# Kernel tuning notes

Hardware: AMD Instinct MI355X
Metric: run time of the kernel (lower is better)

Reference implementation:

```python
import jax, jax.numpy as jnp
import numpy as np

B, S, D = 8, 2048, 512
FF = 2048
E = 8

def setup_inputs() -> dict:
    key = jax.random.key(0)
    ks = jax.random.split(key, 7)
    s = 1.0 / np.sqrt(D)
    sf = 1.0 / np.sqrt(FF)
    return {
        "x":  jax.random.normal(ks[0], (B, S, D), dtype=jnp.float32),
        "Wg": jax.random.uniform(ks[1], (D, E), jnp.float32, -s, s),
        "bg": jax.random.uniform(ks[2], (E,), jnp.float32, -s, s),
        "W1": jax.random.uniform(ks[3], (E, D, FF), jnp.float32, -s, s),
        "b1": jax.random.uniform(ks[4], (E, FF), jnp.float32, -s, s),
        "W2": jax.random.uniform(ks[5], (E, FF, D), jnp.float32, -sf, sf),
        "b2": jax.random.uniform(ks[6], (E, D), jnp.float32, -sf, sf),
    }

def reference(x, Wg, bg, W1, b1, W2, b2):
    b, s, d = x.shape
    xf = x.reshape(-1, d)                      # [T, D]
    logits = xf @ Wg + bg                      # [T, E]
    probs = jax.nn.softmax(logits, axis=-1)
    pmax = jnp.max(probs, axis=-1)             # [T]
    routes = jnp.argmax(probs, axis=-1)        # [T] int
    xs = xf * pmax[:, None]                    # scale tokens by router prob
    # per-expert FFN over all tokens, select the routed expert's output
    out_tok = jnp.zeros_like(xf)
    for e in range(E):
        h = jax.nn.relu(xs @ W1[e] + b1[e])    # [T, FF]
        y = h @ W2[e] + b2[e]                  # [T, D]
        out_tok = jnp.where((routes == e)[:, None], y, out_tok)
    # torch.cat of per-expert nonzero-index gathers == tokens stably sorted by expert id
    order = jnp.argsort(routes)                # jnp.argsort is stable
    return out_tok[order].reshape(b, s, d)
```

## Files before the change

### kernel.cpp

```cpp
#include <hip/hip_runtime.h>
#include <hip/hip_bf16.h>

constexpr int TTOK  = 16384;
constexpr int DDIM  = 512;
constexpr int FFDIM = 2048;
constexpr int NEXP  = 8;
constexpr int GB_TOK = 64;
constexpr int NGB    = TTOK / GB_TOK;
constexpr int MAXTILES = TTOK / 128 + NEXP;

typedef __attribute__((ext_vector_type(8))) short short8_t;
typedef __attribute__((ext_vector_type(4))) float f32x4_t;

__device__ __forceinline__ unsigned short f2bf(float f) {
    union { float f; unsigned u; } v; v.f = f;
    return (unsigned short)((v.u + 0x7fffu + ((v.u >> 16) & 1u)) >> 16);
}

__device__ __forceinline__ void gl_lds16(const void* g, void* l) {
    __builtin_amdgcn_global_load_lds(
        (const __attribute__((address_space(1))) void*)g,
        (__attribute__((address_space(3))) void*)l,
        16, 0, 0);
}

__global__ __launch_bounds__(256) void transpose_cvt(const float* __restrict__ src,
                                                     unsigned short* __restrict__ dst,
                                                     int R, int C) {
    __shared__ float tile[32][33];
    int e = blockIdx.z;
    int c0 = blockIdx.x * 32;
    int r0 = blockIdx.y * 32;
    const float* s = src + (size_t)e * R * C;
    unsigned short* d = dst + (size_t)e * R * C;
    int tx = threadIdx.x, ty = threadIdx.y;
    #pragma unroll
    for (int i = 0; i < 4; i++)
        tile[ty + 8 * i][tx] = s[(size_t)(r0 + ty + 8 * i) * C + c0 + tx];
    __syncthreads();
    #pragma unroll
    for (int i = 0; i < 4; i++)
        d[(size_t)(c0 + ty + 8 * i) * R + r0 + tx] = f2bf(tile[tx][ty + 8 * i]);
}

__global__ __launch_bounds__(256) void gate_kernel(const float* __restrict__ x,
                                                   const float* __restrict__ Wg,
                                                   const float* __restrict__ bg,
                                                   int* __restrict__ route,
                                                   float* __restrict__ pmax,
                                                   int* __restrict__ blockCounts) {
    __shared__ int cnt[NEXP];
    __shared__ float bgs[NEXP];
    int tid = threadIdx.x;
    if (tid < NEXP) { cnt[tid] = 0; bgs[tid] = bg[tid]; }
    __syncthreads();
    int wave = tid >> 6, lane = tid & 63;
    float w[8][8];
    #pragma unroll
    for (int jj = 0; jj < 8; jj++) {
        float4 a = *(const float4*)(Wg + (size_t)(lane * 8 + jj) * NEXP);
        float4 b = *(const float4*)(Wg + (size_t)(lane * 8 + jj) * NEXP + 4);
        w[jj][0] = a.x; w[jj][1] = a.y; w[jj][2] = a.z; w[jj][3] = a.w;
        w[jj][4] = b.x; w[jj][5] = b.y; w[jj][6] = b.z; w[jj][7] = b.w;
    }
    int tbase = blockIdx.x * GB_TOK + wave * 16;
    for (int it = 0; it < 16; it++) {
        int t = tbase + it;
        float4 xa = *(const float4*)(x + (size_t)t * DDIM + lane * 8);
        float4 xb = *(const float4*)(x + (size_t)t * DDIM + lane * 8 + 4);
        float xs[8] = {xa.x, xa.y, xa.z, xa.w, xb.x, xb.y, xb.z, xb.w};
        double acc[NEXP];
        #pragma unroll
        for (int e = 0; e < NEXP; e++) acc[e] = 0.0;
        #pragma unroll
        for (int jj = 0; jj < 8; jj++) {
            double xv = (double)xs[jj];
            #pragma unroll
            for (int e = 0; e < NEXP; e++) acc[e] += xv * (double)w[jj][e];
        }
        #pragma unroll
        for (int off = 32; off > 0; off >>= 1) {
            #pragma unroll
            for (int e = 0; e < NEXP; e++) acc[e] += __shfl_down(acc[e], off);
        }
        if (lane == 0) {
            double l[NEXP];
            #pragma unroll
            for (int e = 0; e < NEXP; e++) l[e] = acc[e] + (double)bgs[e];
            int r = 0; double lm = l[0];
            #pragma unroll
            for (int e = 1; e < NEXP; e++) if (l[e] > lm) { lm = l[e]; r = e; }
            double s = 0.0;
            #pragma unroll
            for (int e = 0; e < NEXP; e++) s += exp(l[e] - lm);
            route[t] = r;
            pmax[t] = (float)(1.0 / s);
            atomicAdd(&cnt[r], 1);
        }
    }
    __syncthreads();
    if (tid < NEXP) blockCounts[blockIdx.x * NEXP + tid] = cnt[tid];
}

__global__ __launch_bounds__(NGB) void scan_kernel(const int* __restrict__ blockCounts,
                                                   int* __restrict__ blockOffsets,
                                                   int* __restrict__ segPrefix,
                                                   int* __restrict__ tilePrefix) {
    __shared__ int sc[NGB][NEXP];
    __shared__ int base[NEXP + 1];
    int b = threadIdx.x;
    int c[NEXP];
    #pragma unroll
    for (int e = 0; e < NEXP; e++) { c[e] = blockCounts[b * NEXP + e]; sc[b][e] = c[e]; }
    __syncthreads();
    for (int off = 1; off < NGB; off <<= 1) {
        int t[NEXP];
        if (b >= off) {
            #pragma unroll
            for (int e = 0; e < NEXP; e++) t[e] = sc[b - off][e];
        }
        __syncthreads();
        if (b >= off) {
            #pragma unroll
            for (int e = 0; e < NEXP; e++) sc[b][e] += t[e];
        }
        __syncthreads();
    }
    if (b == 0) {
        int s = 0;
        #pragma unroll
        for (int e = 0; e < NEXP; e++) { base[e] = s; s += sc[NGB - 1][e]; }
        base[NEXP] = s;
        for (int e = 0; e <= NEXP; e++) segPrefix[e] = base[e];
        int tp = 0;
        tilePrefix[0] = 0;
        for (int e = 0; e < NEXP; e++) {
            tp += (sc[NGB - 1][e] + 127) / 128;
            tilePrefix[e + 1] = tp;
        }
    }
    __syncthreads();
    #pragma unroll
    for (int e = 0; e < NEXP; e++)
        blockOffsets[b * NEXP + e] = base[e] + sc[b][e] - c[e];
}

__global__ __launch_bounds__(256) void scatter_kernel(const float* __restrict__ x,
                                                      const int* __restrict__ route,
                                                      const float* __restrict__ pmax,
                                                      const int* __restrict__ blockOffsets,
                                                      unsigned short* __restrict__ Xs) {
    __shared__ int dstL[GB_TOK];
    __shared__ float pmL[GB_TOK];
    int tid = threadIdx.x;
    int bb = blockIdx.x;
    if (tid < 64) {
        int t = bb * GB_TOK + tid;
        int r = route[t];
        unsigned long long ltmask = (tid == 0) ? 0ull : ((~0ull) >> (64 - tid));
        int rank = 0;
        #pragma unroll
        for (int e = 0; e < NEXP; e++) {
            unsigned long long m = __ballot(r == e);
            if (r == e) rank = __popcll(m & ltmask);
        }
        dstL[tid] = blockOffsets[bb * NEXP + r] + rank;
        pmL[tid] = pmax[t];
    }
    __syncthreads();
    int wave = tid >> 6, lane = tid & 63;
    for (int rr = 0; rr < 16; rr++) {
        int rowl = wave * 16 + rr;
        int t = bb * GB_TOK + rowl;
        float pm = pmL[rowl];
        const float4* xr = (const float4*)(x + (size_t)t * DDIM) + lane * 2;
        float4 a = xr[0], b = xr[1];
        union { short8_t v; unsigned short s[8]; } o;
        o.s[0] = f2bf(a.x * pm); o.s[1] = f2bf(a.y * pm);
        o.s[2] = f2bf(a.z * pm); o.s[3] = f2bf(a.w * pm);
        o.s[4] = f2bf(b.x * pm); o.s[5] = f2bf(b.y * pm);
        o.s[6] = f2bf(b.z * pm); o.s[7] = f2bf(b.w * pm);
        *(short8_t*)(Xs + (size_t)dstL[rowl] * DDIM + lane * 8) = o.v;
    }
}

template <bool RELU, bool BIAS, typename OutT>
__global__ __launch_bounds__(256) void gemm_seg(const unsigned short* __restrict__ A,
                                                const unsigned short* __restrict__ Bt,
                                                const float* __restrict__ bias,
                                                OutT* __restrict__ C,
                                                const int* __restrict__ segPrefix,
                                                const int* __restrict__ tilePrefix,
                                                int K, int N, int kLen) {
    int t = blockIdx.x;
    if (t >= tilePrefix[NEXP]) return;
    int e = 0;
    #pragma unroll
    for (int i = 1; i <= NEXP; i++) e += (t >= tilePrefix[i]) ? 1 : 0;
    int seg1 = segPrefix[e + 1];
    int m0 = segPrefix[e] + (t - tilePrefix[e]) * 128;
    int n0 = blockIdx.y * 128;
    int kc0 = blockIdx.z * kLen;
    C += (size_t)blockIdx.z * TTOK * N;

    __shared__ unsigned short As[2 * 4096];
    __shared__ unsigned short Bs[2 * 4096];

    int tid = threadIdx.x, wave = tid >> 6, lane = tid & 63;
    const unsigned short* Bte = Bt + (size_t)e * N * K;

    int srow = lane >> 2;
    int scol = (lane & 3) * 8;

    f32x4_t acc[4][4];
    #pragma unroll
    for (int i = 0; i < 4; i++)
        #pragma unroll
        for (int j = 0; j < 4; j++) acc[i][j] = (f32x4_t){0.f, 0.f, 0.f, 0.f};

    int wm = (wave & 1) * 64;
    int wn = (wave >> 1) * 64;
    int frow = lane & 15;
    int fk = (lane >> 4) * 8;

    for (int kc = 0; kc < kLen; kc += 64) {
        int kg = kc0 + kc;
        #pragma unroll
        for (int p = 0; p < 2; p++) {
            #pragma unroll
            for (int i = 0; i < 2; i++) {
                int reg = wave * 2 + i;
                int arow = m0 + reg * 16 + srow;
                arow = arow < TTOK ? arow : TTOK - 1;
                gl_lds16(A + (size_t)arow * K + kg + p * 32 + scol, &As[p * 4096 + reg * 512]);
                int brow = n0 + reg * 16 + srow;
                gl_lds16(Bte + (size_t)brow * K + kg + p * 32 + scol, &Bs[p * 4096 + reg * 512]);
            }
        }
        __syncthreads();
        #pragma unroll
        for (int p = 0; p < 2; p++) {
            short8_t af[4], bfr[4];
            #pragma unroll
            for (int i = 0; i < 4; i++)
                af[i] = *(const short8_t*)&As[p * 4096 + (wm + i * 16 + frow) * 32 + fk];
            #pragma unroll
            for (int j = 0; j < 4; j++)
                bfr[j] = *(const short8_t*)&Bs[p * 4096 + (wn + j * 16 + frow) * 32 + fk];
            #pragma unroll
            for (int i = 0; i < 4; i++)
                #pragma unroll
                for (int j = 0; j < 4; j++)
                    acc[i][j] = __builtin_amdgcn_mfma_f32_16x16x32_bf16(af[i], bfr[j], acc[i][j], 0, 0, 0);
        }
        __syncthreads();
    }

    int quad = lane >> 4;
    int colb = lane & 15;
    #pragma unroll
    for (int i = 0; i < 4; i++) {
        #pragma unroll
        for (int j = 0; j < 4; j++) {
            int col = n0 + wn + j * 16 + colb;
            float bv = BIAS ? bias[(size_t)e * N + col] : 0.0f;
            #pragma unroll
            for (int r = 0; r < 4; r++) {
                int row = m0 + wm + i * 16 + quad * 4 + r;
                if (row < seg1) {
                    float v = acc[i][j][r] + bv;
                    if (RELU) v = fmaxf(v, 0.0f);
                    if constexpr (sizeof(OutT) == 2) {
                        C[(size_t)row * N + col] = (OutT)f2bf(v);
                    } else {
                        C[(size_t)row * N + col] = v;
                    }
                }
            }
        }
    }
}

__global__ __launch_bounds__(256) void reduce_add(const float* __restrict__ part,
                                                  const float* __restrict__ b2,
                                                  const int* __restrict__ segPrefix,
                                                  float* __restrict__ out) {
    __shared__ int sp[NEXP + 1];
    if (threadIdx.x <= NEXP) sp[threadIdx.x] = segPrefix[threadIdx.x];
    __syncthreads();
    int wave = threadIdx.x >> 6, lane = threadIdx.x & 63;
    int row = blockIdx.x * 4 + wave;
    int e = 0;
    #pragma unroll
    for (int i = 1; i < NEXP; i++) e += (row >= sp[i]) ? 1 : 0;
    const float4* p0 = (const float4*)(part + (size_t)row * DDIM) + lane * 2;
    const float4* p1 = (const float4*)(part + (size_t)(TTOK + row) * DDIM) + lane * 2;
    const float4* bv = (const float4*)(b2 + (size_t)e * DDIM) + lane * 2;
    float4* o = (float4*)(out + (size_t)row * DDIM) + lane * 2;
    #pragma unroll
    for (int k = 0; k < 2; k++) {
        float4 a = p0[k], b = p1[k], c = bv[k];
        o[k] = make_float4(a.x + b.x + c.x, a.y + b.y + c.y,
                           a.z + b.z + c.z, a.w + b.w + c.w);
    }
}

extern "C" void kernel_launch(void* const* d_in, const int* in_sizes, int n_in,
                              void* d_out, int out_size, void* d_ws, size_t ws_size,
                              hipStream_t stream) {
    const float* x  = (const float*)d_in[0];
    const float* Wg = (const float*)d_in[1];
    const float* bg = (const float*)d_in[2];
    const float* W1 = (const float*)d_in[3];
    const float* b1 = (const float*)d_in[4];
    const float* W2 = (const float*)d_in[5];
    const float* b2 = (const float*)d_in[6];
    float* out = (float*)d_out;

    char* ws = (char*)d_ws;
    size_t off = 0;
    auto alloc = [&](size_t bytes) -> char* {
        char* p = ws + off;
        off += (bytes + 255) & ~(size_t)255;
        return p;
    };
    unsigned short* W1T = (unsigned short*)alloc((size_t)NEXP * DDIM * FFDIM * 2);
    unsigned short* W2T = (unsigned short*)alloc((size_t)NEXP * DDIM * FFDIM * 2);
    unsigned short* Xs  = (unsigned short*)alloc((size_t)TTOK * DDIM * 2);
    unsigned short* H   = (unsigned short*)alloc((size_t)TTOK * FFDIM * 2);
    int*   route        = (int*)alloc((size_t)TTOK * 4);
    float* pmaxArr      = (float*)alloc((size_t)TTOK * 4);
    int*   blockCounts  = (int*)alloc((size_t)NGB * NEXP * 4);
    int*   blockOffsets = (int*)alloc((size_t)NGB * NEXP * 4);
    int*   segPrefix    = (int*)alloc((size_t)(NEXP + 1) * 4);
    int*   tilePrefix   = (int*)alloc((size_t)(NEXP + 1) * 4);
    size_t baseBytes = off;
    float* part = (float*)alloc((size_t)2 * TTOK * DDIM * 4);
    bool doSplit = (off <= ws_size);
    if (!doSplit) off = baseBytes;

    transpose_cvt<<<dim3(FFDIM / 32, DDIM / 32, NEXP), dim3(32, 8), 0, stream>>>(W1, W1T, DDIM, FFDIM);
    transpose_cvt<<<dim3(DDIM / 32, FFDIM / 32, NEXP), dim3(32, 8), 0, stream>>>(W2, W2T, FFDIM, DDIM);
    gate_kernel<<<NGB, 256, 0, stream>>>(x, Wg, bg, route, pmaxArr, blockCounts);
    scan_kernel<<<1, NGB, 0, stream>>>(blockCounts, blockOffsets, segPrefix, tilePrefix);
    scatter_kernel<<<NGB, 256, 0, stream>>>(x, route, pmaxArr, blockOffsets, Xs);
    gemm_seg<true, true, unsigned short><<<dim3(MAXTILES, FFDIM / 128, 1), 256, 0, stream>>>(
        Xs, W1T, b1, H, segPrefix, tilePrefix, DDIM, FFDIM, DDIM);
    if (doSplit) {
        gemm_seg<false, false, float><<<dim3(MAXTILES, DDIM / 128, 2), 256, 0, stream>>>(
            H, W2T, nullptr, part, segPrefix, tilePrefix, FFDIM, DDIM, FFDIM / 2);
        reduce_add<<<TTOK / 4, 256, 0, stream>>>(part, b2, segPrefix, out);
    } else {
        gemm_seg<false, true, float><<<dim3(MAXTILES, DDIM / 128, 1), 256, 0, stream>>>(
            H, W2T, b2, out, segPrefix, tilePrefix, FFDIM, DDIM, FFDIM);
    }
}
```

Before: 329.7 us.

## Drop split-K in second GEMM, use 128x64 tiles and swizzle LDS

```diff
diff --git a/kernel.cpp b/kernel.cpp
--- a/kernel.cpp
+++ b/kernel.cpp
@@ -5,7 +5,7 @@
 constexpr int DDIM  = 512;
 constexpr int FFDIM = 2048;
 constexpr int NEXP  = 8;
-constexpr int GB_TOK = 64;
+constexpr int GB_TOK = 16;
 constexpr int NGB    = TTOK / GB_TOK;
 constexpr int MAXTILES = TTOK / 128 + NEXP;
 
@@ -63,8 +63,8 @@
         w[jj][0] = a.x; w[jj][1] = a.y; w[jj][2] = a.z; w[jj][3] = a.w;
         w[jj][4] = b.x; w[jj][5] = b.y; w[jj][6] = b.z; w[jj][7] = b.w;
     }
-    int tbase = blockIdx.x * GB_TOK + wave * 16;
-    for (int it = 0; it < 16; it++) {
+    int tbase = blockIdx.x * GB_TOK + wave * 4;
+    for (int it = 0; it < 4; it++) {
         int t = tbase + it;
         float4 xa = *(const float4*)(x + (size_t)t * DDIM + lane * 8);
         float4 xb = *(const float4*)(x + (size_t)t * DDIM + lane * 8 + 4);
@@ -102,10 +102,10 @@
     if (tid < NEXP) blockCounts[blockIdx.x * NEXP + tid] = cnt[tid];
 }
 
-__global__ __launch_bounds__(NGB) void scan_kernel(const int* __restrict__ blockCounts,
-                                                   int* __restrict__ blockOffsets,
-                                                   int* __restrict__ segPrefix,
-                                                   int* __restrict__ tilePrefix) {
+__global__ __launch_bounds__(1024) void scan_kernel(const int* __restrict__ blockCounts,
+                                                    int* __restrict__ blockOffsets,
+                                                    int* __restrict__ segPrefix,
+                                                    int* __restrict__ tilePrefix) {
     __shared__ int sc[NGB][NEXP];
     __shared__ int base[NEXP + 1];
     int b = threadIdx.x;
@@ -154,7 +154,7 @@
     __shared__ float pmL[GB_TOK];
     int tid = threadIdx.x;
     int bb = blockIdx.x;
-    if (tid < 64) {
+    if (tid < GB_TOK) {
         int t = bb * GB_TOK + tid;
         int r = route[t];
         unsigned long long ltmask = (tid == 0) ? 0ull : ((~0ull) >> (64 - tid));
@@ -169,8 +169,8 @@
     }
     __syncthreads();
     int wave = tid >> 6, lane = tid & 63;
-    for (int rr = 0; rr < 16; rr++) {
-        int rowl = wave * 16 + rr;
+    for (int rr = 0; rr < 4; rr++) {
+        int rowl = wave * 4 + rr;
         int t = bb * GB_TOK + rowl;
         float pm = pmL[rowl];
         const float4* xr = (const float4*)(x + (size_t)t * DDIM) + lane * 2;
@@ -184,14 +184,16 @@
     }
 }
 
-template <bool RELU, bool BIAS, typename OutT>
+template <bool RELU, int NT, typename OutT>
 __global__ __launch_bounds__(256) void gemm_seg(const unsigned short* __restrict__ A,
                                                 const unsigned short* __restrict__ Bt,
                                                 const float* __restrict__ bias,
                                                 OutT* __restrict__ C,
                                                 const int* __restrict__ segPrefix,
                                                 const int* __restrict__ tilePrefix,
-                                                int K, int N, int kLen) {
+                                                int K, int N) {
+    constexpr int MI   = (NT == 128) ? 4 : 2;
+    constexpr int BPAN = (NT / 16) * 512;
     int t = blockIdx.x;
     if (t >= tilePrefix[NEXP]) return;
     int e = 0;
@@ -199,32 +201,31 @@
     for (int i = 1; i <= NEXP; i++) e += (t >= tilePrefix[i]) ? 1 : 0;
     int seg1 = segPrefix[e + 1];
     int m0 = segPrefix[e] + (t - tilePrefix[e]) * 128;
-    int n0 = blockIdx.y * 128;
-    int kc0 = blockIdx.z * kLen;
-    C += (size_t)blockIdx.z * TTOK * N;
+    int n0 = blockIdx.y * NT;
 
     __shared__ unsigned short As[2 * 4096];
-    __shared__ unsigned short Bs[2 * 4096];
+    __shared__ unsigned short Bs[2 * BPAN];
 
     int tid = threadIdx.x, wave = tid >> 6, lane = tid & 63;
     const unsigned short* Bte = Bt + (size_t)e * N * K;
 
     int srow = lane >> 2;
-    int scol = (lane & 3) * 8;
-
-    f32x4_t acc[4][4];
-    #pragma unroll
-    for (int i = 0; i < 4; i++)
+    int sg   = (lane & 3) ^ ((lane >> 2) & 3) ^ ((lane >> 4) & 3);
+    int scol = sg * 8;
+
+    f32x4_t acc[MI][4];
+    #pragma unroll
+    for (int i = 0; i < MI; i++)
         #pragma unroll
         for (int j = 0; j < 4; j++) acc[i][j] = (f32x4_t){0.f, 0.f, 0.f, 0.f};
 
-    int wm = (wave & 1) * 64;
-    int wn = (wave >> 1) * 64;
+    int wm = (NT == 128) ? ((wave & 1) * 64) : (wave * 32);
+    int wn = (NT == 128) ? ((wave >> 1) * 64) : 0;
     int frow = lane & 15;
-    int fk = (lane >> 4) * 8;
-
-    for (int kc = 0; kc < kLen; kc += 64) {
-        int kg = kc0 + kc;
+    int gr = lane >> 4;
+    int fswz = (gr ^ (frow & 3) ^ ((frow >> 2) & 3)) * 8;
+
+    for (int kc = 0; kc < K; kc += 64) {
         #pragma unroll
         for (int p = 0; p < 2; p++) {
             #pragma unroll
@@ -232,23 +233,33 @@
                 int reg = wave * 2 + i;
                 int arow = m0 + reg * 16 + srow;
                 arow = arow < TTOK ? arow : TTOK - 1;
-                gl_lds16(A + (size_t)arow * K + kg + p * 32 + scol, &As[p * 4096 + reg * 512]);
+                gl_lds16(A + (size_t)arow * K + kc + p * 32 + scol, &As[p * 4096 + reg * 512]);
+            }
+            if (NT == 128) {
+                #pragma unroll
+                for (int i = 0; i < 2; i++) {
+                    int reg = wave * 2 + i;
+                    int brow = n0 + reg * 16 + srow;
+                    gl_lds16(Bte + (size_t)brow * K + kc + p * 32 + scol, &Bs[p * BPAN + reg * 512]);
+                }
+            } else {
+                int reg = wave;
                 int brow = n0 + reg * 16 + srow;
-                gl_lds16(Bte + (size_t)brow * K + kg + p * 32 + scol, &Bs[p * 4096 + reg * 512]);
+                gl_lds16(Bte + (size_t)brow * K + kc + p * 32 + scol, &Bs[p * BPAN + reg * 512]);
             }
         }
         __syncthreads();
         #pragma unroll
         for (int p = 0; p < 2; p++) {
-            short8_t af[4], bfr[4];
-            #pragma unroll
-            for (int i = 0; i < 4; i++)
-                af[i] = *(const short8_t*)&As[p * 4096 + (wm + i * 16 + frow) * 32 + fk];
+            short8_t af[MI], bfr[4];
+            #pragma unroll
+            for (int i = 0; i < MI; i++)
+                af[i] = *(const short8_t*)&As[p * 4096 + (wm + i * 16 + frow) * 32 + fswz];
             #pragma unroll
             for (int j = 0; j < 4; j++)
-                bfr[j] = *(const short8_t*)&Bs[p * 4096 + (wn + j * 16 + frow) * 32 + fk];
-            #pragma unroll
-            for (int i = 0; i < 4; i++)
+                bfr[j] = *(const short8_t*)&Bs[p * BPAN + (wn + j * 16 + frow) * 32 + fswz];
+            #pragma unroll
+            for (int i = 0; i < MI; i++)
                 #pragma unroll
                 for (int j = 0; j < 4; j++)
                     acc[i][j] = __builtin_amdgcn_mfma_f32_16x16x32_bf16(af[i], bfr[j], acc[i][j], 0, 0, 0);
@@ -259,11 +270,11 @@
     int quad = lane >> 4;
     int colb = lane & 15;
     #pragma unroll
-    for (int i = 0; i < 4; i++) {
+    for (int i = 0; i < MI; i++) {
         #pragma unroll
         for (int j = 0; j < 4; j++) {
             int col = n0 + wn + j * 16 + colb;
-            float bv = BIAS ? bias[(size_t)e * N + col] : 0.0f;
+            float bv = bias[(size_t)e * N + col];
             #pragma unroll
             for (int r = 0; r < 4; r++) {
                 int row = m0 + wm + i * 16 + quad * 4 + r;
@@ -278,30 +289,6 @@
                 }
             }
         }
-    }
-}
-
-__global__ __launch_bounds__(256) void reduce_add(const float* __restrict__ part,
-                                                  const float* __restrict__ b2,
-                                                  const int* __restrict__ segPrefix,
-                                                  float* __restrict__ out) {
-    __shared__ int sp[NEXP + 1];
-    if (threadIdx.x <= NEXP) sp[threadIdx.x] = segPrefix[threadIdx.x];
-    __syncthreads();
-    int wave = threadIdx.x >> 6, lane = threadIdx.x & 63;
-    int row = blockIdx.x * 4 + wave;
-    int e = 0;
-    #pragma unroll
-    for (int i = 1; i < NEXP; i++) e += (row >= sp[i]) ? 1 : 0;
-    const float4* p0 = (const float4*)(part + (size_t)row * DDIM) + lane * 2;
-    const float4* p1 = (const float4*)(part + (size_t)(TTOK + row) * DDIM) + lane * 2;
-    const float4* bv = (const float4*)(b2 + (size_t)e * DDIM) + lane * 2;
-    float4* o = (float4*)(out + (size_t)row * DDIM) + lane * 2;
-    #pragma unroll
-    for (int k = 0; k < 2; k++) {
-        float4 a = p0[k], b = p1[k], c = bv[k];
-        o[k] = make_float4(a.x + b.x + c.x, a.y + b.y + c.y,
-                           a.z + b.z + c.z, a.w + b.w + c.w);
     }
 }
 
@@ -334,24 +321,14 @@
     int*   blockOffsets = (int*)alloc((size_t)NGB * NEXP * 4);
     int*   segPrefix    = (int*)alloc((size_t)(NEXP + 1) * 4);
     int*   tilePrefix   = (int*)alloc((size_t)(NEXP + 1) * 4);
-    size_t baseBytes = off;
-    float* part = (float*)alloc((size_t)2 * TTOK * DDIM * 4);
-    bool doSplit = (off <= ws_size);
-    if (!doSplit) off = baseBytes;
 
     transpose_cvt<<<dim3(FFDIM / 32, DDIM / 32, NEXP), dim3(32, 8), 0, stream>>>(W1, W1T, DDIM, FFDIM);
     transpose_cvt<<<dim3(DDIM / 32, FFDIM / 32, NEXP), dim3(32, 8), 0, stream>>>(W2, W2T, FFDIM, DDIM);
     gate_kernel<<<NGB, 256, 0, stream>>>(x, Wg, bg, route, pmaxArr, blockCounts);
     scan_kernel<<<1, NGB, 0, stream>>>(blockCounts, blockOffsets, segPrefix, tilePrefix);
     scatter_kernel<<<NGB, 256, 0, stream>>>(x, route, pmaxArr, blockOffsets, Xs);
-    gemm_seg<true, true, unsigned short><<<dim3(MAXTILES, FFDIM / 128, 1), 256, 0, stream>>>(
-        Xs, W1T, b1, H, segPrefix, tilePrefix, DDIM, FFDIM, DDIM);
-    if (doSplit) {
-        gemm_seg<false, false, float><<<dim3(MAXTILES, DDIM / 128, 2), 256, 0, stream>>>(
-            H, W2T, nullptr, part, segPrefix, tilePrefix, FFDIM, DDIM, FFDIM / 2);
-        reduce_add<<<TTOK / 4, 256, 0, stream>>>(part, b2, segPrefix, out);
-    } else {
-        gemm_seg<false, true, float><<<dim3(MAXTILES, DDIM / 128, 1), 256, 0, stream>>>(
-            H, W2T, b2, out, segPrefix, tilePrefix, FFDIM, DDIM, FFDIM);
-    }
-}
+    gemm_seg<true, 128, unsigned short><<<dim3(MAXTILES, FFDIM / 128, 1), 256, 0, stream>>>(
+        Xs, W1T, b1, H, segPrefix, tilePrefix, DDIM, FFDIM);
+    gemm_seg<false, 64, float><<<dim3(MAXTILES, DDIM / 64, 1), 256, 0, stream>>>(
+        H, W2T, b2, out, segPrefix, tilePrefix, FFDIM, DDIM);
+}
```

Result: no change. 332.6 us (+0.9%).
